# Kernel optimization log

Hardware: AMD Instinct MI355X
Metric: run time of the kernel (lower is better)

## Reference

```python
import jax, jax.numpy as jnp
import numpy as np

LN_EPS = 1e-5

def setup_inputs() -> dict:
    key = jax.random.key(0)
    ks = jax.random.split(key, 10)
    N, E, H, V, L, OUT, G = 100000, 600000, 128, 65, 4, 32, 64
    x_tokens = jax.random.randint(ks[0], (N, 2), 0, V, dtype=jnp.int32)
    edge_index = jax.random.randint(ks[1], (2, E), 0, N, dtype=jnp.int32)
    batch = jnp.sort(jax.random.randint(ks[2], (N,), 0, G)).astype(jnp.int64)
    s = 0.05
    key_emb = jax.random.normal(ks[3], (V, H), jnp.float32) * s
    val_emb = jax.random.normal(ks[4], (V, H), jnp.float32) * s
    Ws = jax.random.normal(ks[5], (L, H, H), jnp.float32) * (1.0 / np.sqrt(H))
    bs = jax.random.normal(ks[6], (L, H), jnp.float32) * s
    ln_g = jnp.ones((L, H), jnp.float32)
    ln_b = jnp.zeros((L, H), jnp.float32)
    out_W = jax.random.normal(ks[7], (OUT, H), jnp.float32) * (1.0 / np.sqrt(H))
    return {"x_tokens": x_tokens, "edge_index": edge_index, "batch": batch,
            "key_emb": key_emb, "val_emb": val_emb, "Ws": Ws, "bs": bs,
            "ln_g": ln_g, "ln_b": ln_b, "out_W": out_W}

def _layer_norm(x, g, b):
    mu = jnp.mean(x, axis=-1, keepdims=True)
    var = jnp.mean(jnp.square(x - mu), axis=-1, keepdims=True)
    return (x - mu) * jax.lax.rsqrt(var + LN_EPS) * g + b

def reference(x_tokens, edge_index, batch, key_emb, val_emb, Ws, bs, ln_g, ln_b, out_W):
    N = x_tokens.shape[0]
    L = Ws.shape[0]
    # layer-0: key + value embedding lookup -> [N, H]
    x = key_emb[x_tokens[:, 0]] + val_emb[x_tokens[:, 1]]
    # GCN normalization with self-loops (computed once; edges fixed per layer)
    loop = jnp.arange(N, dtype=edge_index.dtype)
    src = jnp.concatenate([edge_index[0], loop])  # [E+N]
    dst = jnp.concatenate([edge_index[1], loop])
    deg = jax.ops.segment_sum(jnp.ones_like(dst, dtype=x.dtype), dst, num_segments=N)
    dis = jnp.where(deg > 0, jax.lax.rsqrt(jnp.maximum(deg, 1.0)), 0.0)
    norm = (dis[src] * dis[dst])[:, None]  # [E+N, 1]
    for i in range(L):
        xw = x @ Ws[i]  # [N, H]
        agg = jax.ops.segment_sum(norm * xw[src], dst, num_segments=N) + bs[i]
        new_x = jax.nn.relu(agg)          # use_activation
        x = x + new_x                      # use_residual
        x = _layer_norm(x, ln_g[i], ln_b[i])  # use_layer_norm
    logits = x @ out_W.T  # Linear(bias=False) -> [N, out_dim]
    return logits
```

## Files before the change

### kernel.cpp

```cpp
#include <hip/hip_runtime.h>

#define H 128
#define LN_EPS 1e-5f

typedef unsigned short u16;
typedef unsigned int u32;
typedef __attribute__((ext_vector_type(8))) short bf16x8;
typedef __attribute__((ext_vector_type(4))) float f32x4;

__device__ __forceinline__ float bflo(u32 u){ return __uint_as_float(u << 16); }
__device__ __forceinline__ float bfhi(u32 u){ return __uint_as_float(u & 0xFFFF0000u); }
__device__ __forceinline__ float bf1(u16 u){ return __uint_as_float(((u32)u) << 16); }
__device__ __forceinline__ u16 f2bu(float f){
  u32 u = __float_as_uint(f);
  return (u16)((u + 0x7FFFu + ((u >> 16) & 1u)) >> 16);
}

__device__ __forceinline__ float ldf(const void* p, int i, bool isbf){
  return isbf ? bf1(reinterpret_cast<const u16*>(p)[i])
              : reinterpret_cast<const float*>(p)[i];
}


__global__ void k_convert(const void* __restrict__ kemb, const void* __restrict__ vemb,
                          const void* __restrict__ Ws,   const void* __restrict__ bs,
                          const void* __restrict__ lng,  const void* __restrict__ lnb,
                          const void* __restrict__ outW,
                          float* __restrict__ kemb_f, float* __restrict__ vemb_f,
                          u16* __restrict__ W_c, float* __restrict__ bs_f,
                          float* __restrict__ lng_f, float* __restrict__ lnb_f,
                          u16* __restrict__ outW_b, int* __restrict__ flag,
                          int V, int L, int OUT){
  bool isbf = (*reinterpret_cast<const u32*>(lng) == 0x3F803F80u);
  if (blockIdx.x == 0 && threadIdx.x == 0) flag[0] = isbf ? 1 : 0;
  int i = blockIdx.x * blockDim.x + threadIdx.x;
  int nEmb = V * H;
  int nW   = L * H * H;
  int nVec = L * H;
  int nOut = OUT * H;
  if (i < nEmb){ kemb_f[i] = ldf(kemb, i, isbf); vemb_f[i] = ldf(vemb, i, isbf); }
  if (i < nW){
    int j = i & 7, lane = (i >> 3) & 63, g = i >> 9;
    int s = g & 3, cg = (g >> 2) & 7, l = g >> 5;
    int k = s * 32 + (lane >> 4) * 8 + j;
    int n = cg * 16 + (lane & 15);
    W_c[i] = f2bu(ldf(Ws, l * H * H + k * H + n, isbf));
  }
  if (i < nVec){ bs_f[i] = ldf(bs, i, isbf); lng_f[i] = ldf(lng, i, isbf);
                 lnb_f[i] = ldf(lnb, i, isbf); }
  if (i < nOut){ outW_b[i] = f2bu(ldf(outW, i, isbf)); }
}


__global__ void k_count(const int* __restrict__ dst, int E, int* __restrict__ deg){
  int i = blockIdx.x * blockDim.x + threadIdx.x;
  if (i < E) atomicAdd(&deg[dst[i]], 1);
}

__device__ __forceinline__ int paddedLen(int d){ return (d + 4) & ~3; }

__global__ void k_bsum(const int* __restrict__ deg, int* __restrict__ bsum, int N){
  __shared__ int sh[256];
  int i = blockIdx.x * 256 + threadIdx.x;
  sh[threadIdx.x] = (i < N) ? paddedLen(deg[i]) : 0;
  __syncthreads();
  for (int off = 128; off > 0; off >>= 1){
    if (threadIdx.x < off) sh[threadIdx.x] += sh[threadIdx.x + off];
    __syncthreads();
  }
  if (threadIdx.x == 0) bsum[blockIdx.x] = sh[0];
}

__global__ void k_bscan(int* __restrict__ bsum, int nb){
  __shared__ int sh[1024];
  int t = threadIdx.x;
  sh[t] = (t < nb) ? bsum[t] : 0;
  __syncthreads();
  for (int off = 1; off < 1024; off <<= 1){
    int add = (t >= off) ? sh[t - off] : 0;
    __syncthreads();
    sh[t] += add;
    __syncthreads();
  }
  if (t < nb) bsum[t] = (t > 0) ? sh[t - 1] : 0;
}

__global__ void k_scan2(const int* __restrict__ deg, const int* __restrict__ bsum,
                        int* __restrict__ row_ptr, float* __restrict__ dis,
                        int* __restrict__ cursor, int2* __restrict__ csr, int N){
  __shared__ int sh[256];
  int i = blockIdx.x * 256 + threadIdx.x;
  int d = (i < N) ? deg[i] : 0;
  int v = (i < N) ? paddedLen(d) : 0;
  sh[threadIdx.x] = v;
  __syncthreads();
  for (int off = 1; off < 256; off <<= 1){
    int add = (threadIdx.x >= off) ? sh[threadIdx.x - off] : 0;
    __syncthreads();
    sh[threadIdx.x] += add;
    __syncthreads();
  }
  int excl = sh[threadIdx.x] - v + bsum[blockIdx.x];
  if (i < N){
    row_ptr[i] = excl;
    float r = rsqrtf((float)(d + 1));
    dis[i] = r;
    cursor[i] = 1;
    csr[excl] = make_int2(i * (H / 2), __float_as_int(r * r));
    for (int p = excl + d + 1; p < excl + v; p++)
      csr[p] = make_int2(0, 0);
  }
  if (i == N - 1) row_ptr[N] = excl + v;
}

__global__ void k_fill(const int* __restrict__ src, const int* __restrict__ dst, int E,
                       const float* __restrict__ dis, const int* __restrict__ row_ptr,
                       int* __restrict__ cursor, int2* __restrict__ csr){
  int i = blockIdx.x * blockDim.x + threadIdx.x;
  if (i >= E) return;
  int s = src[i], d = dst[i];
  int pos = atomicAdd(&cursor[d], 1);
  csr[row_ptr[d] + pos] = make_int2(s * (H / 2), __float_as_int(dis[s] * dis[d]));
}


__global__ __launch_bounds__(256) void k_embed(const int* __restrict__ tok,
                        const float* __restrict__ kemb, const float* __restrict__ vemb,
                        u16* __restrict__ xb, int N){
  int n = blockIdx.x * 4 + (threadIdx.x >> 6);
  if (n >= N) return;
  int h0 = (threadIdx.x & 63) * 2;
  int t0 = tok[n * 2], t1 = tok[n * 2 + 1];
  float2 k2 = *reinterpret_cast<const float2*>(&kemb[t0 * H + h0]);
  float2 v2 = *reinterpret_cast<const float2*>(&vemb[t1 * H + h0]);
  *reinterpret_cast<u32*>(&xb[(size_t)n * H + h0]) =
      (u32)f2bu(k2.x + v2.x) | ((u32)f2bu(k2.y + v2.y) << 16);
}


__global__ __launch_bounds__(256) void k_gemm(const u16* __restrict__ xb,
                                              const u16* __restrict__ Wc,
                                              u16* __restrict__ xw, int npairs){
  int wid = threadIdx.x >> 6, lane = threadIdx.x & 63;
  int sp = wid >> 1;
  int ch = wid & 1;
  int r = lane & 15, kq = lane >> 4;
  bf16x8 wf[4][4];
  #pragma unroll
  for (int c = 0; c < 4; c++)
    #pragma unroll
    for (int s = 0; s < 4; s++)
      wf[c][s] = *reinterpret_cast<const bf16x8*>(
          Wc + (size_t)((((ch * 4 + c) * 4 + s) * 64 + lane) << 3));
  for (int p = blockIdx.x; p < npairs; p += gridDim.x){
    int node0 = (p * 2 + sp) << 4;
    const u16* xrow = xb + (size_t)node0 * H + r * H + kq * 8;
    bf16x8 xf[4];
    #pragma unroll
    for (int s = 0; s < 4; s++)
      xf[s] = *reinterpret_cast<const bf16x8*>(xrow + s * 32);
    f32x4 acc[4] = {{0,0,0,0},{0,0,0,0},{0,0,0,0},{0,0,0,0}};
    #pragma unroll
    for (int s = 0; s < 4; s++)
      #pragma unroll
      for (int c = 0; c < 4; c++)
        acc[c] = __builtin_amdgcn_mfma_f32_16x16x32_bf16(wf[c][s], xf[s], acc[c], 0, 0, 0);
    u16* orow = xw + (size_t)(node0 + r) * H + ch * 64 + kq * 4;
    #pragma unroll
    for (int c = 0; c < 4; c++){
      u32 lo = (u32)f2bu(acc[c][0]) | ((u32)f2bu(acc[c][1]) << 16);
      u32 hi = (u32)f2bu(acc[c][2]) | ((u32)f2bu(acc[c][3]) << 16);
      *reinterpret_cast<uint2*>(orow + c * 16) = make_uint2(lo, hi);
    }
  }
}


__global__ __launch_bounds__(256) void k_gather(const u32* __restrict__ xw32,
    const int* __restrict__ row_ptr, const int2* __restrict__ csr,
    const float* __restrict__ bias, const float* __restrict__ gamma,
    const float* __restrict__ beta,
    u16* __restrict__ xb, int N){
  int lane = threadIdx.x & 63;
  int w = blockIdx.x * 4 + (threadIdx.x >> 6);
  int n0 = w * 2;
  if (n0 >= N) return;
  bool two = (n0 + 1 < N);
  int h0 = lane * 2;
  int rs0 = __builtin_amdgcn_readfirstlane(row_ptr[n0]);
  int rm  = __builtin_amdgcn_readfirstlane(row_ptr[n0 + 1]);
  int re1 = two ? __builtin_amdgcn_readfirstlane(row_ptr[n0 + 2]) : rm;
  int len0 = rm - rs0, len1 = re1 - rm;
  int common = min(len0, len1);
  u32 xv0 = *reinterpret_cast<const u32*>(&xb[(size_t)n0 * H + h0]);
  u32 xv1 = two ? *reinterpret_cast<const u32*>(&xb[(size_t)(n0 + 1) * H + h0]) : 0u;
  float2 b2 = *reinterpret_cast<const float2*>(&bias[h0]);
  float2 g2 = *reinterpret_cast<const float2*>(&gamma[h0]);
  float2 t2 = *reinterpret_cast<const float2*>(&beta[h0]);
  float a00 = 0.f, a01 = 0.f, a10 = 0.f, a11 = 0.f;
#define EDGE(c, A0, A1) { \
    u32 cx = (u32)__builtin_amdgcn_readfirstlane(c.x); \
    float wgt = __uint_as_float((u32)__builtin_amdgcn_readfirstlane(c.y)); \
    u32 v = xw32[cx + lane]; \
    A0 = fmaf(wgt, bflo(v), A0); A1 = fmaf(wgt, bfhi(v), A1); }
  int i = 0;
  for (; i < common; i += 4){
    int2 c0 = csr[rs0+i], c1 = csr[rs0+i+1], c2 = csr[rs0+i+2], c3 = csr[rs0+i+3];
    int2 d0 = csr[rm+i],  d1 = csr[rm+i+1],  d2 = csr[rm+i+2],  d3 = csr[rm+i+3];
    EDGE(c0,a00,a01) EDGE(d0,a10,a11) EDGE(c1,a00,a01) EDGE(d1,a10,a11)
    EDGE(c2,a00,a01) EDGE(d2,a10,a11) EDGE(c3,a00,a01) EDGE(d3,a10,a11)
  }
  for (; i < len0; i += 4){
    int2 c0 = csr[rs0+i], c1 = csr[rs0+i+1], c2 = csr[rs0+i+2], c3 = csr[rs0+i+3];
    EDGE(c0,a00,a01) EDGE(c1,a00,a01) EDGE(c2,a00,a01) EDGE(c3,a00,a01)
  }
  for (; i < len1; i += 4){
    int2 d0 = csr[rm+i], d1 = csr[rm+i+1], d2 = csr[rm+i+2], d3 = csr[rm+i+3];
    EDGE(d0,a10,a11) EDGE(d1,a10,a11) EDGE(d2,a10,a11) EDGE(d3,a10,a11)
  }
#undef EDGE
  float v0 = fmaxf(a00 + b2.x, 0.f), v1 = fmaxf(a01 + b2.y, 0.f);
  v0 += bflo(xv0); v1 += bfhi(xv0);
  float u0 = fmaxf(a10 + b2.x, 0.f), u1 = fmaxf(a11 + b2.y, 0.f);
  u0 += bflo(xv1); u1 += bfhi(xv1);
  float s0 = v0 + v1, s1 = u0 + u1;
  #pragma unroll
  for (int off = 32; off > 0; off >>= 1){
    s0 += __shfl_xor(s0, off);
    s1 += __shfl_xor(s1, off);
  }
  float mu0 = s0 * (1.f / 128.f), mu1 = s1 * (1.f / 128.f);
  float d00 = v0 - mu0, d01 = v1 - mu0;
  float d10 = u0 - mu1, d11 = u1 - mu1;
  float q0 = d00 * d00 + d01 * d01, q1 = d10 * d10 + d11 * d11;
  #pragma unroll
  for (int off = 32; off > 0; off >>= 1){
    q0 += __shfl_xor(q0, off);
    q1 += __shfl_xor(q1, off);
  }
  float inv0 = rsqrtf(q0 * (1.f / 128.f) + LN_EPS);
  float inv1 = rsqrtf(q1 * (1.f / 128.f) + LN_EPS);
  float o00 = d00 * inv0 * g2.x + t2.x, o01 = d01 * inv0 * g2.y + t2.y;
  *reinterpret_cast<u32*>(&xb[(size_t)n0 * H + h0]) =
      (u32)f2bu(o00) | ((u32)f2bu(o01) << 16);
  if (two){
    float o10 = d10 * inv1 * g2.x + t2.x, o11 = d11 * inv1 * g2.y + t2.y;
    *reinterpret_cast<u32*>(&xb[(size_t)(n0+1) * H + h0]) =
        (u32)f2bu(o10) | ((u32)f2bu(o11) << 16);
  }
}


__global__ __launch_bounds__(256) void k_out(const u16* __restrict__ xb,
    const u16* __restrict__ oWb, u16* __restrict__ out16, float* __restrict__ outf,
    const int* __restrict__ flag, int nstrips){
  int wid = threadIdx.x >> 6, lane = threadIdx.x & 63;
  int r = lane & 15, kq = lane >> 4;
  bool isbf = (flag[0] != 0);
  bf16x8 wf[2][4];
  #pragma unroll
  for (int ct = 0; ct < 2; ct++)
    #pragma unroll
    for (int s = 0; s < 4; s++)
      wf[ct][s] = *reinterpret_cast<const bf16x8*>(
          oWb + (ct * 16 + r) * H + s * 32 + kq * 8);
  for (int strip = blockIdx.x * 4 + wid; strip < nstrips; strip += gridDim.x * 4){
    const u16* xrow = xb + (size_t)strip * 16 * H + r * H + kq * 8;
    bf16x8 xf[4];
    #pragma unroll
    for (int s = 0; s < 4; s++)
      xf[s] = *reinterpret_cast<const bf16x8*>(xrow + s * 32);
    f32x4 acc[2] = {{0,0,0,0},{0,0,0,0}};
    #pragma unroll
    for (int s = 0; s < 4; s++)
      #pragma unroll
      for (int ct = 0; ct < 2; ct++)
        acc[ct] = __builtin_amdgcn_mfma_f32_16x16x32_bf16(wf[ct][s], xf[s], acc[ct], 0, 0, 0);
    int node = strip * 16 + r;
    if (isbf){
      #pragma unroll
      for (int ct = 0; ct < 2; ct++){
        u32 lo = (u32)f2bu(acc[ct][0]) | ((u32)f2bu(acc[ct][1]) << 16);
        u32 hi = (u32)f2bu(acc[ct][2]) | ((u32)f2bu(acc[ct][3]) << 16);
        *reinterpret_cast<uint2*>(out16 + (size_t)node * 32 + ct * 16 + kq * 4) =
            make_uint2(lo, hi);
      }
    } else {
      #pragma unroll
      for (int ct = 0; ct < 2; ct++)
        *reinterpret_cast<f32x4*>(outf + (size_t)node * 32 + ct * 16 + kq * 4) = acc[ct];
    }
  }
}


extern "C" void kernel_launch(void* const* d_in, const int* in_sizes, int n_in,
                              void* d_out, int out_size, void* d_ws, size_t ws_size,
                              hipStream_t stream){
  const int*  x_tokens = (const int*)d_in[0];
  const int*  edge_idx = (const int*)d_in[1];
  const void* kemb = d_in[3];
  const void* vemb = d_in[4];
  const void* Ws   = d_in[5];
  const void* bs   = d_in[6];
  const void* lng  = d_in[7];
  const void* lnb  = d_in[8];
  const void* outW = d_in[9];

  int N   = in_sizes[0] / 2;
  int E   = in_sizes[1] / 2;
  int V   = in_sizes[3] / H;
  int L   = in_sizes[5] / (H * H);
  int OUT = in_sizes[9] / H;

  char* ws = (char*)d_ws;
  size_t off = 0;
  auto alloc = [&](size_t bytes) -> void* {
    void* p = ws + off;
    off += (bytes + 255) & ~(size_t)255;
    return p;
  };
  u16*   xb     = (u16*)  alloc((size_t)N * H * 2);
  u16*   xw     = (u16*)  alloc((size_t)N * H * 2);
  int*   deg    = (int*)  alloc((size_t)N * 4);
  int*   cursor = (int*)  alloc((size_t)N * 4);
  int*   row_ptr= (int*)  alloc((size_t)(N + 1) * 4);
  float* dis    = (float*)alloc((size_t)N * 4);
  int*   bsum   = (int*)  alloc(1024 * 4);
  int2*  csr    = (int2*) alloc(((size_t)E + 4 * (size_t)N) * 8);
  float* kemb_f = (float*)alloc((size_t)V * H * 4);
  float* vemb_f = (float*)alloc((size_t)V * H * 4);
  u16*   W_c    = (u16*)  alloc((size_t)L * H * H * 2);
  float* bs_f   = (float*)alloc((size_t)L * H * 4);
  float* lng_f  = (float*)alloc((size_t)L * H * 4);
  float* lnb_f  = (float*)alloc((size_t)L * H * 4);
  u16*   outW_b = (u16*)  alloc((size_t)OUT * H * 2);
  int*   flag   = (int*)  alloc(256);

  const int* esrc = edge_idx;
  const int* edst = edge_idx + E;

  (void)hipMemsetAsync(deg, 0, (size_t)N * 4, stream);

  int convTotal = L * H * H;
  int cb = (convTotal + 255) / 256;
  k_convert<<<cb, 256, 0, stream>>>(kemb, vemb, Ws, bs, lng, lnb, outW,
                                    kemb_f, vemb_f, W_c, bs_f, lng_f, lnb_f,
                                    outW_b, flag, V, L, OUT);

  int eb = (E + 255) / 256;
  int nb = (N + 255) / 256;
  k_count<<<eb, 256, 0, stream>>>(edst, E, deg);
  k_bsum <<<nb, 256, 0, stream>>>(deg, bsum, N);
  k_bscan<<<1, 1024, 0, stream>>>(bsum, nb);
  k_scan2<<<nb, 256, 0, stream>>>(deg, bsum, row_ptr, dis, cursor, csr, N);
  k_fill <<<eb, 256, 0, stream>>>(esrc, edst, E, dis, row_ptr, cursor, csr);
  k_embed<<<(N + 3) / 4, 256, 0, stream>>>(x_tokens, kemb_f, vemb_f, xb, N);

  int nstrips = N / 16;
  int npairs  = nstrips / 2;
  int gwaves  = (N + 1) / 2;
  for (int l = 0; l < L; l++){
    k_gemm  <<<1024, 256, 0, stream>>>(xb, W_c + (size_t)l * H * H, xw, npairs);
    k_gather<<<(gwaves + 3) / 4, 256, 0, stream>>>((const u32*)xw, row_ptr, csr,
                                                   bs_f + l * H, lng_f + l * H,
                                                   lnb_f + l * H, xb, N);
  }
  k_out<<<512, 256, 0, stream>>>(xb, outW_b, (u16*)d_out, (float*)d_out, flag, nstrips);
}
```

Measured before the change: 313.4 us.

## Replace CSR prefix scan with atomic row allocation and unroll gather deeper

Replaces the three-kernel prefix scan (block sum, block scan, scan2) with a single kernel that claims each row's padded CSR segment through a global atomic counter, storing start/end pairs per row. The gather reads both rows' bounds with one int4 load and adds an 8-edge unrolled loop to keep more loads in flight. Also sets launch_bounds minimum blocks on k_gemm and changes the k_out grid size. Atomic allocation removes two launches but gives non-monotonic row placement, which can hurt locality of CSR reads in the gather.

```diff
diff --git a/kernel.cpp b/kernel.cpp
--- a/kernel.cpp
+++ b/kernel.cpp
@@ -52,75 +52,40 @@
 }
 
 
-__global__ void k_count(const int* __restrict__ dst, int E, int* __restrict__ deg){
+__global__ void k_count(const int* __restrict__ dst, int E, int* __restrict__ deg,
+                        int* __restrict__ gcur){
   int i = blockIdx.x * blockDim.x + threadIdx.x;
+  if (i == 0) gcur[0] = 0;
   if (i < E) atomicAdd(&deg[dst[i]], 1);
 }
 
 __device__ __forceinline__ int paddedLen(int d){ return (d + 4) & ~3; }
 
-__global__ void k_bsum(const int* __restrict__ deg, int* __restrict__ bsum, int N){
-  __shared__ int sh[256];
-  int i = blockIdx.x * 256 + threadIdx.x;
-  sh[threadIdx.x] = (i < N) ? paddedLen(deg[i]) : 0;
-  __syncthreads();
-  for (int off = 128; off > 0; off >>= 1){
-    if (threadIdx.x < off) sh[threadIdx.x] += sh[threadIdx.x + off];
-    __syncthreads();
-  }
-  if (threadIdx.x == 0) bsum[blockIdx.x] = sh[0];
-}
-
-__global__ void k_bscan(int* __restrict__ bsum, int nb){
-  __shared__ int sh[1024];
-  int t = threadIdx.x;
-  sh[t] = (t < nb) ? bsum[t] : 0;
-  __syncthreads();
-  for (int off = 1; off < 1024; off <<= 1){
-    int add = (t >= off) ? sh[t - off] : 0;
-    __syncthreads();
-    sh[t] += add;
-    __syncthreads();
-  }
-  if (t < nb) bsum[t] = (t > 0) ? sh[t - 1] : 0;
-}
-
-__global__ void k_scan2(const int* __restrict__ deg, const int* __restrict__ bsum,
-                        int* __restrict__ row_ptr, float* __restrict__ dis,
+__global__ void k_alloc(const int* __restrict__ deg, int* __restrict__ gcur,
+                        int2* __restrict__ rowinfo, float* __restrict__ dis,
                         int* __restrict__ cursor, int2* __restrict__ csr, int N){
-  __shared__ int sh[256];
-  int i = blockIdx.x * 256 + threadIdx.x;
-  int d = (i < N) ? deg[i] : 0;
-  int v = (i < N) ? paddedLen(d) : 0;
-  sh[threadIdx.x] = v;
-  __syncthreads();
-  for (int off = 1; off < 256; off <<= 1){
-    int add = (threadIdx.x >= off) ? sh[threadIdx.x - off] : 0;
-    __syncthreads();
-    sh[threadIdx.x] += add;
-    __syncthreads();
-  }
-  int excl = sh[threadIdx.x] - v + bsum[blockIdx.x];
-  if (i < N){
-    row_ptr[i] = excl;
-    float r = rsqrtf((float)(d + 1));
-    dis[i] = r;
-    cursor[i] = 1;
-    csr[excl] = make_int2(i * (H / 2), __float_as_int(r * r));
-    for (int p = excl + d + 1; p < excl + v; p++)
-      csr[p] = make_int2(0, 0);
-  }
-  if (i == N - 1) row_ptr[N] = excl + v;
+  int i = blockIdx.x * blockDim.x + threadIdx.x;
+  if (i >= N) return;
+  int d = deg[i];
+  int padded = paddedLen(d);
+  int base = atomicAdd(gcur, padded);
+  rowinfo[i] = make_int2(base, base + padded);
+  float r = rsqrtf((float)(d + 1));
+  dis[i] = r;
+  cursor[i] = 1;
+  csr[base] = make_int2(i * (H / 2), __float_as_int(r * r));
+  for (int p = base + d + 1; p < base + padded; p++)
+    csr[p] = make_int2(0, 0);
 }
 
 __global__ void k_fill(const int* __restrict__ src, const int* __restrict__ dst, int E,
-                       const float* __restrict__ dis, const int* __restrict__ row_ptr,
+                       const float* __restrict__ dis, const int2* __restrict__ rowinfo,
                        int* __restrict__ cursor, int2* __restrict__ csr){
   int i = blockIdx.x * blockDim.x + threadIdx.x;
   if (i >= E) return;
   int s = src[i], d = dst[i];
   int pos = atomicAdd(&cursor[d], 1);
-  csr[row_ptr[d] + pos] = make_int2(s * (H / 2), __float_as_int(dis[s] * dis[d]));
+  csr[rowinfo[d].x + pos] = make_int2(s * (H / 2), __float_as_int(dis[s] * dis[d]));
 }
 
 
@@ -138,9 +103,9 @@
 }
 
 
-__global__ __launch_bounds__(256) void k_gemm(const u16* __restrict__ xb,
-                                              const u16* __restrict__ Wc,
-                                              u16* __restrict__ xw, int npairs){
+__global__ __launch_bounds__(256, 1) void k_gemm(const u16* __restrict__ xb,
+                                                 const u16* __restrict__ Wc,
+                                                 u16* __restrict__ xw, int npairs){
   int wid = threadIdx.x >> 6, lane = threadIdx.x & 63;
   int sp = wid >> 1;
   int ch = wid & 1;
@@ -177,7 +142,7 @@
 
 
 __global__ __launch_bounds__(256) void k_gather(const u32* __restrict__ xw32,
-    const int* __restrict__ row_ptr, const int2* __restrict__ csr,
+    const int2* __restrict__ rowinfo, const int2* __restrict__ csr,
     const float* __restrict__ bias, const float* __restrict__ gamma,
     const float* __restrict__ beta,
     u16* __restrict__ xb, int N){
@@ -187,10 +152,20 @@
   if (n0 >= N) return;
   bool two = (n0 + 1 < N);
   int h0 = lane * 2;
-  int rs0 = __builtin_amdgcn_readfirstlane(row_ptr[n0]);
-  int rm  = __builtin_amdgcn_readfirstlane(row_ptr[n0 + 1]);
-  int re1 = two ? __builtin_amdgcn_readfirstlane(row_ptr[n0 + 2]) : rm;
-  int len0 = rm - rs0, len1 = re1 - rm;
+  int rs0, re0, rs1, re1;
+  if (two){
+    int4 ri = *reinterpret_cast<const int4*>(&rowinfo[n0]);
+    rs0 = __builtin_amdgcn_readfirstlane(ri.x);
+    re0 = __builtin_amdgcn_readfirstlane(ri.y);
+    rs1 = __builtin_amdgcn_readfirstlane(ri.z);
+    re1 = __builtin_amdgcn_readfirstlane(ri.w);
+  } else {
+    int2 ri = rowinfo[n0];
+    rs0 = __builtin_amdgcn_readfirstlane(ri.x);
+    re0 = __builtin_amdgcn_readfirstlane(ri.y);
+    rs1 = rs0; re1 = rs0;
+  }
+  int len0 = re0 - rs0, len1 = re1 - rs1;
   int common = min(len0, len1);
   u32 xv0 = *reinterpret_cast<const u32*>(&xb[(size_t)n0 * H + h0]);
   u32 xv1 = two ? *reinterpret_cast<const u32*>(&xb[(size_t)(n0 + 1) * H + h0]) : 0u;
@@ -204,9 +179,19 @@
     u32 v = xw32[cx + lane]; \
     A0 = fmaf(wgt, bflo(v), A0); A1 = fmaf(wgt, bfhi(v), A1); }
   int i = 0;
+  for (; i + 8 <= common; i += 8){
+    int2 c0 = csr[rs0+i],   c1 = csr[rs0+i+1], c2 = csr[rs0+i+2], c3 = csr[rs0+i+3];
+    int2 c4 = csr[rs0+i+4], c5 = csr[rs0+i+5], c6 = csr[rs0+i+6], c7 = csr[rs0+i+7];
+    int2 d0 = csr[rs1+i],   d1 = csr[rs1+i+1], d2 = csr[rs1+i+2], d3 = csr[rs1+i+3];
+    int2 d4 = csr[rs1+i+4], d5 = csr[rs1+i+5], d6 = csr[rs1+i+6], d7 = csr[rs1+i+7];
+    EDGE(c0,a00,a01) EDGE(d0,a10,a11) EDGE(c1,a00,a01) EDGE(d1,a10,a11)
+    EDGE(c2,a00,a01) EDGE(d2,a10,a11) EDGE(c3,a00,a01) EDGE(d3,a10,a11)
+    EDGE(c4,a00,a01) EDGE(d4,a10,a11) EDGE(c5,a00,a01) EDGE(d5,a10,a11)
+    EDGE(c6,a00,a01) EDGE(d6,a10,a11) EDGE(c7,a00,a01) EDGE(d7,a10,a11)
+  }
   for (; i < common; i += 4){
     int2 c0 = csr[rs0+i], c1 = csr[rs0+i+1], c2 = csr[rs0+i+2], c3 = csr[rs0+i+3];
-    int2 d0 = csr[rm+i],  d1 = csr[rm+i+1],  d2 = csr[rm+i+2],  d3 = csr[rm+i+3];
+    int2 d0 = csr[rs1+i], d1 = csr[rs1+i+1], d2 = csr[rs1+i+2], d3 = csr[rs1+i+3];
     EDGE(c0,a00,a01) EDGE(d0,a10,a11) EDGE(c1,a00,a01) EDGE(d1,a10,a11)
     EDGE(c2,a00,a01) EDGE(d2,a10,a11) EDGE(c3,a00,a01) EDGE(d3,a10,a11)
   }
@@ -215,7 +200,7 @@
     EDGE(c0,a00,a01) EDGE(c1,a00,a01) EDGE(c2,a00,a01) EDGE(c3,a00,a01)
   }
   for (; i < len1; i += 4){
-    int2 d0 = csr[rm+i], d1 = csr[rm+i+1], d2 = csr[rm+i+2], d3 = csr[rm+i+3];
+    int2 d0 = csr[rs1+i], d1 = csr[rs1+i+1], d2 = csr[rs1+i+2], d3 = csr[rs1+i+3];
     EDGE(d0,a10,a11) EDGE(d1,a10,a11) EDGE(d2,a10,a11) EDGE(d3,a10,a11)
   }
 #undef EDGE
@@ -324,9 +309,9 @@
   u16*   xw     = (u16*)  alloc((size_t)N * H * 2);
   int*   deg    = (int*)  alloc((size_t)N * 4);
   int*   cursor = (int*)  alloc((size_t)N * 4);
-  int*   row_ptr= (int*)  alloc((size_t)(N + 1) * 4);
+  int2*  rowinfo= (int2*) alloc((size_t)N * 8);
   float* dis    = (float*)alloc((size_t)N * 4);
-  int*   bsum   = (int*)  alloc(1024 * 4);
+  int*   gcur   = (int*)  alloc(256);
   int2*  csr    = (int2*) alloc(((size_t)E + 4 * (size_t)N) * 8);
   float* kemb_f = (float*)alloc((size_t)V * H * 4);
   float* vemb_f = (float*)alloc((size_t)V * H * 4);
@@ -350,11 +335,9 @@
 
   int eb = (E + 255) / 256;
   int nb = (N + 255) / 256;
-  k_count<<<eb, 256, 0, stream>>>(edst, E, deg);
-  k_bsum <<<nb, 256, 0, stream>>>(deg, bsum, N);
-  k_bscan<<<1, 1024, 0, stream>>>(bsum, nb);
-  k_scan2<<<nb, 256, 0, stream>>>(deg, bsum, row_ptr, dis, cursor, csr, N);
-  k_fill <<<eb, 256, 0, stream>>>(esrc, edst, E, dis, row_ptr, cursor, csr);
+  k_count<<<eb, 256, 0, stream>>>(edst, E, deg, gcur);
+  k_alloc<<<nb, 256, 0, stream>>>(deg, gcur, rowinfo, dis, cursor, csr, N);
+  k_fill <<<eb, 256, 0, stream>>>(esrc, edst, E, dis, rowinfo, cursor, csr);
   k_embed<<<(N + 3) / 4, 256, 0, stream>>>(x_tokens, kemb_f, vemb_f, xb, N);
 
   int nstrips = N / 16;
@@ -362,9 +345,10 @@
   int gwaves  = (N + 1) / 2;
   for (int l = 0; l < L; l++){
     k_gemm  <<<1024, 256, 0, stream>>>(xb, W_c + (size_t)l * H * H, xw, npairs);
-    k_gather<<<(gwaves + 3) / 4, 256, 0, stream>>>((const u32*)xw, row_ptr, csr,
+    k_gather<<<(gwaves + 3) / 4, 256, 0, stream>>>((const u32*)xw, rowinfo, csr,
                                                    bs_f + l * H, lng_f + l * H,
                                                    lnb_f + l * H, xb, N);
   }
-  k_out<<<512, 256, 0, stream>>>(xb, outW_b, (u16*)d_out, (float*)d_out, flag, nstrips);
-}
+  k_out<<<(nstrips + 3) / 4, 256, 0, stream>>>(xb, outW_b, (u16*)d_out, (float*)d_out,
+                                               flag, nstrips);
+}
```

Result: slower. 325.4 us (+3.9%).
